# Kernel optimization log

Hardware: AMD Instinct MI355X
Metric: run time of the kernel (lower is better)

Reference implementation:

```python
import jax, jax.numpy as jnp
import numpy as np

DIM = 768
HEADS = 12
HEAD_DIM = DIM // HEADS
SCALE = HEAD_DIM ** -0.5


def setup_inputs() -> dict:
    key = jax.random.key(0)
    k1, k2, k3, k4 = jax.random.split(key, 4)
    x = jax.random.normal(k1, (8, 1025, DIM), dtype=jnp.float32)
    # torch nn.Linear weight layout: (out_features, in_features)
    w_qkv = jax.random.normal(k2, (3 * DIM, DIM), dtype=jnp.float32) * (DIM ** -0.5)
    w_proj = jax.random.normal(k3, (DIM, DIM), dtype=jnp.float32) * (DIM ** -0.5)
    b_proj = jax.random.normal(k4, (DIM,), dtype=jnp.float32) * 0.01
    return {"x": x, "w_qkv": w_qkv, "w_proj": w_proj, "b_proj": b_proj}


def reference(x, w_qkv, w_proj, b_proj):
    B, N, C = x.shape
    H, D = HEADS, HEAD_DIM
    # qkv: (B, N, 3C) -> (3, B, H, N, D)
    qkv = jnp.einsum('bnc,oc->bno', x, w_qkv)
    qkv = qkv.reshape(B, N, 3, H, D).transpose(2, 0, 3, 1, 4)
    q, k, v = qkv[0], qkv[1], qkv[2]
    attn = jnp.einsum('bhnd,bhmd->bhnm', q, k) * SCALE
    attn = jax.nn.softmax(attn, axis=-1)
    out = jnp.einsum('bhnm,bhmd->bhnd', attn, v)
    out = out.transpose(0, 2, 1, 3).reshape(B, N, C)
    out = jnp.einsum('bnc,oc->bno', out, w_proj) + b_proj
    return out
```

## Files before the change

kernel.cpp:

```cpp
#include <hip/hip_runtime.h>
#include <stdint.h>

#define DIMC 768
#define NSEQ 1025
#define BATCH 8
#define HEADS 12
#define HDIM 64
#define OC3 2304
#define MROWS (BATCH * NSEQ)
#define NBH (BATCH * HEADS)
#define KVB 64
#define NT 17
#define QTILE 128
#define NQT 9
#define HTILES 9
#define VSTRIDE (NT * KVB)
#define C2 0.1803368801111244f
#define OFFB (-11.541560327111707f)

typedef short bf16x8 __attribute__((ext_vector_type(8)));
typedef float f32x4 __attribute__((ext_vector_type(4)));
typedef float f32x16 __attribute__((ext_vector_type(16)));
typedef uint32_t u32x4 __attribute__((ext_vector_type(4)));

__device__ __forceinline__ uint32_t f2bf(float x) {
    uint32_t u = __builtin_bit_cast(uint32_t, x);
    return (u + 0x7fffu + ((u >> 16) & 1u)) >> 16;
}
__device__ __forceinline__ float bf2f(uint32_t b) {
    return __builtin_bit_cast(float, b << 16);
}
__device__ __forceinline__ float4 ld4(const float* p) {
    return *reinterpret_cast<const float4*>(p);
}
__device__ __forceinline__ uint32_t cvtpk(float lo, float hi) {
    uint32_t r;
    asm("v_cvt_pk_bf16_f32 %0, %1, %2" : "=v"(r) : "v"(lo), "v"(hi));
    return r;
}
__device__ __forceinline__ void plswap(uint32_t& x, uint32_t& y) {
    asm volatile("v_permlane32_swap_b32 %0, %1" : "+v"(x), "+v"(y));
}
__device__ __forceinline__ void async_cp16(void* lds, const void* g) {
    __builtin_amdgcn_global_load_lds(
        (const __attribute__((address_space(1))) uint32_t*)g,
        (__attribute__((address_space(3))) uint32_t*)lds, 16, 0, 0);
}

__global__ __launch_bounds__(256) void cvt_all(const float* __restrict__ x,
                                               const float* __restrict__ wq,
                                               const float* __restrict__ wp,
                                               uint16_t* __restrict__ xb,
                                               uint16_t* __restrict__ wqb,
                                               uint16_t* __restrict__ wpb) {
    const int NX = MROWS * DIMC / 8, NQ = OC3 * DIMC / 8, NP = DIMC * DIMC / 8;
    const int i = blockIdx.x * 256 + threadIdx.x;
    const float* src;
    uint16_t* dst;
    int off;
    if (i < NX)                { src = x;  dst = xb;  off = i; }
    else if (i < NX + NQ)      { src = wq; dst = wqb; off = i - NX; }
    else if (i < NX + NQ + NP) { src = wp; dst = wpb; off = i - NX - NQ; }
    else return;
    const float4 a = ld4(src + off * 8), b = ld4(src + off * 8 + 4);
    uint4 o;
    o.x = f2bf(a.x) | (f2bf(a.y) << 16);
    o.y = f2bf(a.z) | (f2bf(a.w) << 16);
    o.z = f2bf(b.x) | (f2bf(b.y) << 16);
    o.w = f2bf(b.z) | (f2bf(b.w) << 16);
    *reinterpret_cast<uint4*>(dst + off * 8) = o;
}

template <bool OUTBF, bool BIAS>
__global__ __launch_bounds__(256) void gemm_bf16_nt(const uint16_t* __restrict__ A,
                                                    const uint16_t* __restrict__ W,
                                                    const float* __restrict__ bias,
                                                    void* __restrict__ Out,
                                                    int M, int N, int K) {
    __shared__ __align__(16) char smem[32768];
    char* const As = smem;
    char* const Ws = smem + 16384;

    const int tid = threadIdx.x;
    const int wave = tid >> 6, lane = tid & 63;
    const int l15 = lane & 15, l4 = lane >> 4;
    const int wr = wave >> 1, wc = wave & 1;
    const int m0 = blockIdx.y * 128, n0 = blockIdx.x * 128;

    f32x4 acc[4][4] = {};

    int srow[4], scol[4];
#pragma unroll
    for (int i = 0; i < 4; ++i) {
        const int X = i * 4096 + wave * 1024 + lane * 16;
        const int row = X >> 7;
        const int slot = (X & 127) >> 4;
        srow[i] = row;
        scol[i] = (slot ^ (row & 7)) << 3;
    }

    for (int kt = 0; kt < K; kt += 64) {
        __syncthreads();
#pragma unroll
        for (int i = 0; i < 4; ++i) {
            int am = m0 + srow[i];
            if (am >= M) am = M - 1;
            async_cp16(As + i * 4096 + wave * 1024,
                       A + (size_t)am * K + kt + scol[i]);
            const int wn = n0 + srow[i];
            async_cp16(Ws + i * 4096 + wave * 1024,
                       W + (size_t)wn * K + kt + scol[i]);
        }
        __syncthreads();

#pragma unroll
        for (int ch = 0; ch < 2; ++ch) {
            const int kb = (ch << 6) + (l4 << 4);
            bf16x8 af[4], bw[4];
#pragma unroll
            for (int mi = 0; mi < 4; ++mi) {
                const int row = wr * 64 + mi * 16 + l15;
                af[mi] = *(const bf16x8*)(As + (row << 7) + (kb ^ ((row & 7) << 4)));
            }
#pragma unroll
            for (int nj = 0; nj < 4; ++nj) {
                const int row = wc * 64 + nj * 16 + l15;
                bw[nj] = *(const bf16x8*)(Ws + (row << 7) + (kb ^ ((row & 7) << 4)));
            }
#pragma unroll
            for (int mi = 0; mi < 4; ++mi)
#pragma unroll
                for (int nj = 0; nj < 4; ++nj)
                    acc[mi][nj] = __builtin_amdgcn_mfma_f32_16x16x32_bf16(
                        af[mi], bw[nj], acc[mi][nj], 0, 0, 0);
        }
    }

#pragma unroll
    for (int mi = 0; mi < 4; ++mi) {
#pragma unroll
        for (int r = 0; r < 4; ++r) {
            const int m = m0 + wr * 64 + mi * 16 + l4 * 4 + r;
            if (m < M) {
#pragma unroll
                for (int nj = 0; nj < 4; ++nj) {
                    const int n = n0 + wc * 64 + nj * 16 + l15;
                    float v = acc[mi][nj][r];
                    if (BIAS) v += bias[n];
                    if (OUTBF)
                        ((uint16_t*)Out)[(size_t)m * N + n] = (uint16_t)f2bf(v);
                    else
                        ((float*)Out)[(size_t)m * N + n] = v;
                }
            }
        }
    }
}

__global__ __launch_bounds__(256) void vtrans(const uint16_t* __restrict__ qkv,
                                              uint16_t* __restrict__ vt) {
    const int kt = blockIdx.x, bh = blockIdx.y;
    const int h = bh % HEADS, b = bh / HEADS;
    __shared__ __align__(16) char lds[8192];
    const int tid = threadIdx.x;
    const uint16_t* src = qkv + (size_t)b * NSEQ * OC3 + 2 * DIMC + h * HDIM;
    uint16_t* dst = vt + (size_t)bh * HDIM * VSTRIDE + kt * KVB;

#pragma unroll
    for (int i = 0; i < 2; ++i) {
        const int s = i * 256 + tid;
        const int kv = s >> 3, c = s & 7;
        int kvg = kt * KVB + kv;
        if (kvg > NSEQ - 1) kvg = NSEQ - 1;
        const uint4 d4 = *(const uint4*)(src + (size_t)kvg * OC3 + c * 8);
        *(uint4*)(lds + (kv << 7) + ((c ^ (kv & 7)) << 4)) = d4;
    }
    __syncthreads();

#pragma unroll
    for (int i = 0; i < 2; ++i) {
        const int s = i * 256 + tid;
        const int d = s >> 3, c = s & 7;
        uint32_t w[4];
#pragma unroll
        for (int p = 0; p < 4; ++p) {
            const int k0 = c * 8 + p * 2, k1 = k0 + 1;
            const uint32_t lo = *(const uint16_t*)(lds + (k0 << 7) +
                ((((d >> 3) ^ (k0 & 7)) << 4) + ((d & 7) << 1)));
            const uint32_t hi = *(const uint16_t*)(lds + (k1 << 7) +
                ((((d >> 3) ^ (k1 & 7)) << 4) + ((d & 7) << 1)));
            w[p] = lo | (hi << 16);
        }
        uint4 o4;
        o4.x = w[0]; o4.y = w[1]; o4.z = w[2]; o4.w = w[3];
        *(uint4*)(dst + (size_t)d * VSTRIDE + c * 8) = o4;
    }
}

__global__ __launch_bounds__(256) void flash_attn2(const uint16_t* __restrict__ qkv,
                                                   const uint16_t* __restrict__ vt,
                                                   uint16_t* __restrict__ opart,
                                                   float* __restrict__ lpart) {
    const int wg = blockIdx.x;
    const int lg = (wg & 7) * 216 + (wg >> 3);
    const int qt = lg % NQT;
    const int g = lg / NQT;
    const int bh = g >> 1;
    const int half = g & 1;
    const int h = bh % HEADS, b = bh / HEADS;

    const int tid = threadIdx.x;
    const int wave = tid >> 6, lane = tid & 63;
    const int l31 = lane & 31, lh = lane >> 5;

    __shared__ __align__(16) char smem[32768];

    const uint16_t* Kg = qkv + (size_t)b * NSEQ * OC3 + DIMC + h * HDIM;
    const uint16_t* Vt = vt + (size_t)bh * HDIM * VSTRIDE;

    bf16x8 qf[4];
    {
        int qrow = qt * QTILE + wave * 32 + l31;
        if (qrow > NSEQ - 1) qrow = NSEQ - 1;
        const uint16_t* Qg = qkv + (size_t)(b * NSEQ + qrow) * OC3 + h * HDIM;
#pragma unroll
        for (int ds = 0; ds < 4; ++ds)
            qf[ds] = *(const bf16x8*)(Qg + ds * 16 + lh * 8);
    }

    bf16x8 ones;
#pragma unroll
    for (int i = 0; i < 8; ++i) ones[i] = (short)0x3F80;

    auto stageK = [&](int kv0, char* Kb) {
#pragma unroll
        for (int i = 0; i < 2; ++i) {
            const int X = i * 4096 + wave * 1024 + lane * 16;
            const int row = X >> 7;
            const int slot = (X & 127) >> 4;
            int kvg = kv0 + row;
            if (kvg > NSEQ - 1) kvg = NSEQ - 1;
            async_cp16(Kb + i * 4096 + wave * 1024,
                       Kg + (size_t)kvg * OC3 + ((slot ^ (row & 7)) << 3));
        }
    };
    auto stageV = [&](int kv0, char* Vb) {
#pragma unroll
        for (int i = 0; i < 2; ++i) {
            const int X = i * 4096 + wave * 1024 + lane * 16;
            const int d = X >> 7;
            const int slot = (X & 127) >> 4;
            async_cp16(Vb + i * 4096 + wave * 1024,
                       Vt + (size_t)d * VSTRIDE + kv0 + ((slot ^ (d & 7)) << 3));
        }
    };

    const int tstart = half * HTILES;
    const int tend = half ? NT : HTILES;

    stageK(tstart * KVB, smem);
    stageV(tstart * KVB, smem + 16384);
    __syncthreads();

    f32x16 o[2] = {};
    f32x16 osum = {};

    for (int t = tstart; t < tend; ++t) {
        const int cur = (t - tstart) & 1;
        const int kv0 = t * KVB;
        char* const Kc = smem + cur * 8192;
        char* const Vc = smem + 16384 + cur * 8192;

        if (t < tend - 1) {
            stageK(kv0 + KVB, smem + (cur ^ 1) * 8192);
            stageV(kv0 + KVB, smem + 16384 + (cur ^ 1) * 8192);
        }

        f32x16 s[2] = {};
        __builtin_amdgcn_s_setprio(1);
#pragma unroll
        for (int kvb = 0; kvb < 2; ++kvb) {
            const int krow = kvb * 32 + l31;
            const int kbase = (krow << 7);
            const int sw = (l31 & 7) << 4;
#pragma unroll
            for (int ds = 0; ds < 4; ++ds) {
                bf16x8 kf = *(const bf16x8*)(Kc + kbase + ((ds * 32 + lh * 16) ^ sw));
                s[kvb] = __builtin_amdgcn_mfma_f32_32x32x16_bf16(kf, qf[ds], s[kvb], 0, 0, 0);
            }
        }
        __builtin_amdgcn_s_setprio(0);

        if (t == NT - 1) {
#pragma unroll
            for (int kvb = 0; kvb < 2; ++kvb)
#pragma unroll
                for (int r = 0; r < 16; ++r) {
                    const int kvg = kv0 + kvb * 32 + (r & 3) + 8 * (r >> 2) + 4 * lh;
                    if (kvg >= NSEQ) s[kvb][r] = -INFINITY;
                }
        }

#pragma unroll
        for (int kvb = 0; kvb < 2; ++kvb)
#pragma unroll
            for (int r = 0; r < 16; ++r)
                s[kvb][r] = __builtin_amdgcn_exp2f(fmaf(s[kvb][r], C2, OFFB));

        bf16x8 pa[4];
#pragma unroll
        for (int kb = 0; kb < 4; ++kb) {
            const f32x16 S = s[kb >> 1];
            const int c = (kb & 1) * 8;
            uint32_t w0 = cvtpk(S[c + 0], S[c + 1]);
            uint32_t w2 = cvtpk(S[c + 4], S[c + 5]);
            plswap(w0, w2);
            uint32_t w1 = cvtpk(S[c + 2], S[c + 3]);
            uint32_t w3 = cvtpk(S[c + 6], S[c + 7]);
            plswap(w1, w3);
            u32x4 w;
            w[0] = w0; w[1] = w1; w[2] = w2; w[3] = w3;
            pa[kb] = __builtin_bit_cast(bf16x8, w);
        }

        __builtin_amdgcn_s_setprio(1);
#pragma unroll
        for (int kb = 0; kb < 4; ++kb)
            osum = __builtin_amdgcn_mfma_f32_32x32x16_bf16(ones, pa[kb], osum, 0, 0, 0);
#pragma unroll
        for (int db = 0; db < 2; ++db) {
            const int d = db * 32 + l31;
            const int dbase = (d << 7);
            const int sw = (l31 & 7) << 4;
#pragma unroll
            for (int kb = 0; kb < 4; ++kb) {
                bf16x8 vf = *(const bf16x8*)(Vc + dbase + ((kb * 32 + lh * 16) ^ sw));
                o[db] = __builtin_amdgcn_mfma_f32_32x32x16_bf16(vf, pa[kb], o[db], 0, 0, 0);
            }
        }
        __builtin_amdgcn_s_setprio(0);

        if (t < tend - 1) __syncthreads();
    }

    {
        const int qrow = qt * QTILE + wave * 32 + l31;
        if (qrow < NSEQ) {
            const size_t row = ((size_t)half * NBH + bh) * NSEQ + qrow;
            uint16_t* orow = opart + row * HDIM;
#pragma unroll
            for (int db = 0; db < 2; ++db)
#pragma unroll
                for (int g4 = 0; g4 < 4; ++g4) {
                    const int d = db * 32 + g4 * 8 + lh * 4;
                    uint2 ww;
                    ww.x = cvtpk(o[db][g4 * 4 + 0], o[db][g4 * 4 + 1]);
                    ww.y = cvtpk(o[db][g4 * 4 + 2], o[db][g4 * 4 + 3]);
                    *(uint2*)(orow + d) = ww;
                }
            if (lh == 0) lpart[row] = osum[0];
        }
    }
}

__global__ __launch_bounds__(256) void combine(const uint16_t* __restrict__ opart,
                                               const float* __restrict__ lpart,
                                               uint16_t* __restrict__ attb) {
    const int gid = blockIdx.x * 256 + threadIdx.x;
    if (gid >= NBH * NSEQ * 8) return;
    const int oct = gid & 7;
    const int t = gid >> 3;
    const int bh = t / NSEQ;
    const int q = t - bh * NSEQ;
    const int h = bh % HEADS, b = bh / HEADS;
    const size_t HALF = (size_t)NBH * NSEQ;

    const uint4 o1 = *(const uint4*)(opart + (size_t)t * HDIM + oct * 8);
    const uint4 o2 = *(const uint4*)(opart + (HALF + t) * HDIM + oct * 8);
    const float inv = 1.0f / (lpart[t] + lpart[HALF + t]);

    const uint32_t a[4] = {o1.x, o1.y, o1.z, o1.w};
    const uint32_t c[4] = {o2.x, o2.y, o2.z, o2.w};
    uint2 w0, w1;
    float v[8];
#pragma unroll
    for (int p = 0; p < 4; ++p) {
        v[p * 2 + 0] = (bf2f(a[p] & 0xffffu) + bf2f(c[p] & 0xffffu)) * inv;
        v[p * 2 + 1] = (bf2f(a[p] >> 16) + bf2f(c[p] >> 16)) * inv;
    }
    w0.x = cvtpk(v[0], v[1]); w0.y = cvtpk(v[2], v[3]);
    w1.x = cvtpk(v[4], v[5]); w1.y = cvtpk(v[6], v[7]);

    uint16_t* dst = attb + ((size_t)b * NSEQ + q) * DIMC + h * HDIM + oct * 8;
    *(uint2*)dst = w0;
    *(uint2*)(dst + 4) = w1;
}

extern "C" void kernel_launch(void* const* d_in, const int* in_sizes, int n_in,
                              void* d_out, int out_size, void* d_ws, size_t ws_size,
                              hipStream_t stream) {
    const float* x      = (const float*)d_in[0];
    const float* w_qkv  = (const float*)d_in[1];
    const float* w_proj = (const float*)d_in[2];
    const float* b_proj = (const float*)d_in[3];
    float* out = (float*)d_out;

    const size_t NVT = (size_t)NBH * HDIM * VSTRIDE;
    const size_t NOP = (size_t)2 * NBH * NSEQ * HDIM;
    uint16_t* xb    = (uint16_t*)d_ws;
    uint16_t* wqb   = xb  + (size_t)MROWS * DIMC;
    uint16_t* wpb   = wqb + (size_t)OC3 * DIMC;
    uint16_t* qkv   = wpb + (size_t)DIMC * DIMC;
    uint16_t* vt    = qkv + (size_t)MROWS * OC3;
    uint16_t* opart = vt + NVT;
    float*    lpart = (float*)(opart + NOP);
    uint16_t* attb  = (uint16_t*)(lpart + (size_t)2 * NBH * NSEQ);

    const dim3 blk(256);
    const int ncvt = (MROWS * DIMC + OC3 * DIMC + DIMC * DIMC) / 8;
    cvt_all<<<dim3((ncvt + 255) / 256), blk, 0, stream>>>(x, w_qkv, w_proj, xb, wqb, wpb);

    gemm_bf16_nt<true, false><<<dim3(OC3 / 128, (MROWS + 127) / 128), blk, 0, stream>>>(
        xb, wqb, nullptr, qkv, MROWS, OC3, DIMC);

    vtrans<<<dim3(NT, NBH), blk, 0, stream>>>(qkv, vt);

    flash_attn2<<<dim3(NQT * NBH * 2), blk, 0, stream>>>(qkv, vt, opart, lpart);

    combine<<<dim3((NBH * NSEQ * 8 + 255) / 256), blk, 0, stream>>>(opart, lpart, attb);

    gemm_bf16_nt<false, true><<<dim3(DIMC / 128, (MROWS + 127) / 128), blk, 0, stream>>>(
        attb, wpb, b_proj, out, MROWS, DIMC, DIMC);
}
```

Baseline: 136.1 us.

## Process two 32-row query groups per wave with 128-thread attention blocks

The flash attention kernel now runs 2 waves per block instead of 4, and each wave handles 64 query rows as two 32-row groups. Each K and V fragment read from LDS therefore feeds two MFMAs, halving LDS reads per unit of compute. Staging loops are widened so the two waves still fill the same 128-row tile. The cost is roughly double the accumulator registers per wave and fewer waves per block, which may lower occupancy and reduce latency hiding.

```diff
diff --git a/kernel.cpp b/kernel.cpp
--- a/kernel.cpp
+++ b/kernel.cpp
@@ -197,7 +197,7 @@
     }
 }
 
-__global__ __launch_bounds__(256) void flash_attn2(const uint16_t* __restrict__ qkv,
+__global__ __launch_bounds__(128) void flash_attn2(const uint16_t* __restrict__ qkv,
                                                    const uint16_t* __restrict__ vt,
                                                    uint16_t* __restrict__ opart,
                                                    float* __restrict__ lpart) {
@@ -218,14 +218,15 @@
     const uint16_t* Kg = qkv + (size_t)b * NSEQ * OC3 + DIMC + h * HDIM;
     const uint16_t* Vt = vt + (size_t)bh * HDIM * VSTRIDE;
 
-    bf16x8 qf[4];
-    {
-        int qrow = qt * QTILE + wave * 32 + l31;
+    bf16x8 qf[2][4];
+#pragma unroll
+    for (int G = 0; G < 2; ++G) {
+        int qrow = qt * QTILE + wave * 64 + G * 32 + l31;
         if (qrow > NSEQ - 1) qrow = NSEQ - 1;
         const uint16_t* Qg = qkv + (size_t)(b * NSEQ + qrow) * OC3 + h * HDIM;
 #pragma unroll
         for (int ds = 0; ds < 4; ++ds)
-            qf[ds] = *(const bf16x8*)(Qg + ds * 16 + lh * 8);
+            qf[G][ds] = *(const bf16x8*)(Qg + ds * 16 + lh * 8);
     }
 
     bf16x8 ones;
@@ -234,23 +235,23 @@
 
     auto stageK = [&](int kv0, char* Kb) {
 #pragma unroll
-        for (int i = 0; i < 2; ++i) {
-            const int X = i * 4096 + wave * 1024 + lane * 16;
+        for (int i = 0; i < 4; ++i) {
+            const int X = i * 2048 + wave * 1024 + lane * 16;
             const int row = X >> 7;
             const int slot = (X & 127) >> 4;
             int kvg = kv0 + row;
             if (kvg > NSEQ - 1) kvg = NSEQ - 1;
-            async_cp16(Kb + i * 4096 + wave * 1024,
+            async_cp16(Kb + i * 2048 + wave * 1024,
                        Kg + (size_t)kvg * OC3 + ((slot ^ (row & 7)) << 3));
         }
     };
     auto stageV = [&](int kv0, char* Vb) {
 #pragma unroll
-        for (int i = 0; i < 2; ++i) {
-            const int X = i * 4096 + wave * 1024 + lane * 16;
+        for (int i = 0; i < 4; ++i) {
+            const int X = i * 2048 + wave * 1024 + lane * 16;
             const int d = X >> 7;
             const int slot = (X & 127) >> 4;
-            async_cp16(Vb + i * 4096 + wave * 1024,
+            async_cp16(Vb + i * 2048 + wave * 1024,
                        Vt + (size_t)d * VSTRIDE + kv0 + ((slot ^ (d & 7)) << 3));
         }
     };
@@ -262,8 +263,8 @@
     stageV(tstart * KVB, smem + 16384);
     __syncthreads();
 
-    f32x16 o[2] = {};
-    f32x16 osum = {};
+    f32x16 o[2][2] = {};
+    f32x16 osum[2] = {};
 
     for (int t = tstart; t < tend; ++t) {
         const int cur = (t - tstart) & 1;
@@ -276,7 +277,7 @@
             stageV(kv0 + KVB, smem + 16384 + (cur ^ 1) * 8192);
         }
 
-        f32x16 s[2] = {};
+        f32x16 s[2][2] = {};
         __builtin_amdgcn_s_setprio(1);
 #pragma unroll
         for (int kvb = 0; kvb < 2; ++kvb) {
@@ -286,47 +287,56 @@
 #pragma unroll
             for (int ds = 0; ds < 4; ++ds) {
                 bf16x8 kf = *(const bf16x8*)(Kc + kbase + ((ds * 32 + lh * 16) ^ sw));
-                s[kvb] = __builtin_amdgcn_mfma_f32_32x32x16_bf16(kf, qf[ds], s[kvb], 0, 0, 0);
+                s[0][kvb] = __builtin_amdgcn_mfma_f32_32x32x16_bf16(kf, qf[0][ds], s[0][kvb], 0, 0, 0);
+                s[1][kvb] = __builtin_amdgcn_mfma_f32_32x32x16_bf16(kf, qf[1][ds], s[1][kvb], 0, 0, 0);
             }
         }
         __builtin_amdgcn_s_setprio(0);
 
         if (t == NT - 1) {
 #pragma unroll
+            for (int G = 0; G < 2; ++G)
+#pragma unroll
+                for (int kvb = 0; kvb < 2; ++kvb)
+#pragma unroll
+                    for (int r = 0; r < 16; ++r) {
+                        const int kvg = kv0 + kvb * 32 + (r & 3) + 8 * (r >> 2) + 4 * lh;
+                        if (kvg >= NSEQ) s[G][kvb][r] = -INFINITY;
+                    }
+        }
+
+#pragma unroll
+        for (int G = 0; G < 2; ++G)
+#pragma unroll
             for (int kvb = 0; kvb < 2; ++kvb)
 #pragma unroll
-                for (int r = 0; r < 16; ++r) {
-                    const int kvg = kv0 + kvb * 32 + (r & 3) + 8 * (r >> 2) + 4 * lh;
-                    if (kvg >= NSEQ) s[kvb][r] = -INFINITY;
-                }
-        }
-
-#pragma unroll
-        for (int kvb = 0; kvb < 2; ++kvb)
-#pragma unroll
-            for (int r = 0; r < 16; ++r)
-                s[kvb][r] = __builtin_amdgcn_exp2f(fmaf(s[kvb][r], C2, OFFB));
-
-        bf16x8 pa[4];
+                for (int r = 0; r < 16; ++r)
+                    s[G][kvb][r] = __builtin_amdgcn_exp2f(fmaf(s[G][kvb][r], C2, OFFB));
+
+        bf16x8 pa[2][4];
+#pragma unroll
+        for (int G = 0; G < 2; ++G)
+#pragma unroll
+            for (int kb = 0; kb < 4; ++kb) {
+                const f32x16 S = s[G][kb >> 1];
+                const int c = (kb & 1) * 8;
+                uint32_t w0 = cvtpk(S[c + 0], S[c + 1]);
+                uint32_t w2 = cvtpk(S[c + 4], S[c + 5]);
+                plswap(w0, w2);
+                uint32_t w1 = cvtpk(S[c + 2], S[c + 3]);
+                uint32_t w3 = cvtpk(S[c + 6], S[c + 7]);
+                plswap(w1, w3);
+                u32x4 w;
+                w[0] = w0; w[1] = w1; w[2] = w2; w[3] = w3;
+                pa[G][kb] = __builtin_bit_cast(bf16x8, w);
+            }
+
+        __builtin_amdgcn_s_setprio(1);
 #pragma unroll
         for (int kb = 0; kb < 4; ++kb) {
-            const f32x16 S = s[kb >> 1];
-            const int c = (kb & 1) * 8;
-            uint32_t w0 = cvtpk(S[c + 0], S[c + 1]);
-            uint32_t w2 = cvtpk(S[c + 4], S[c + 5]);
-            plswap(w0, w2);
-            uint32_t w1 = cvtpk(S[c + 2], S[c + 3]);
-            uint32_t w3 = cvtpk(S[c + 6], S[c + 7]);
-            plswap(w1, w3);
-            u32x4 w;
-            w[0] = w0; w[1] = w1; w[2] = w2; w[3] = w3;
-            pa[kb] = __builtin_bit_cast(bf16x8, w);
-        }
-
-        __builtin_amdgcn_s_setprio(1);
-#pragma unroll
-        for (int kb = 0; kb < 4; ++kb)
-            osum = __builtin_amdgcn_mfma_f32_32x32x16_bf16(ones, pa[kb], osum, 0, 0, 0);
+            osum[0] = __builtin_amdgcn_mfma_f32_32x32x16_bf16(ones, pa[0][kb], osum[0], 0, 0, 0);
+            osum[1] = __builtin_amdgcn_mfma_f32_32x32x16_bf16(ones, pa[1][kb], osum[1], 0, 0, 0);
+        }
 #pragma unroll
         for (int db = 0; db < 2; ++db) {
             const int d = db * 32 + l31;
@@ -335,7 +345,8 @@
 #pragma unroll
             for (int kb = 0; kb < 4; ++kb) {
                 bf16x8 vf = *(const bf16x8*)(Vc + dbase + ((kb * 32 + lh * 16) ^ sw));
-                o[db] = __builtin_amdgcn_mfma_f32_32x32x16_bf16(vf, pa[kb], o[db], 0, 0, 0);
+                o[0][db] = __builtin_amdgcn_mfma_f32_32x32x16_bf16(vf, pa[0][kb], o[0][db], 0, 0, 0);
+                o[1][db] = __builtin_amdgcn_mfma_f32_32x32x16_bf16(vf, pa[1][kb], o[1][db], 0, 0, 0);
             }
         }
         __builtin_amdgcn_s_setprio(0);
@@ -343,8 +354,9 @@
         if (t < tend - 1) __syncthreads();
     }
 
-    {
-        const int qrow = qt * QTILE + wave * 32 + l31;
+#pragma unroll
+    for (int G = 0; G < 2; ++G) {
+        const int qrow = qt * QTILE + wave * 64 + G * 32 + l31;
         if (qrow < NSEQ) {
             const size_t row = ((size_t)half * NBH + bh) * NSEQ + qrow;
             uint16_t* orow = opart + row * HDIM;
@@ -354,11 +366,11 @@
                 for (int g4 = 0; g4 < 4; ++g4) {
                     const int d = db * 32 + g4 * 8 + lh * 4;
                     uint2 ww;
-                    ww.x = cvtpk(o[db][g4 * 4 + 0], o[db][g4 * 4 + 1]);
-                    ww.y = cvtpk(o[db][g4 * 4 + 2], o[db][g4 * 4 + 3]);
+                    ww.x = cvtpk(o[G][db][g4 * 4 + 0], o[G][db][g4 * 4 + 1]);
+                    ww.y = cvtpk(o[G][db][g4 * 4 + 2], o[G][db][g4 * 4 + 3]);
                     *(uint2*)(orow + d) = ww;
                 }
-            if (lh == 0) lpart[row] = osum[0];
+            if (lh == 0) lpart[row] = osum[G][0];
         }
     }
 }
@@ -425,7 +437,7 @@
 
     vtrans<<<dim3(NT, NBH), blk, 0, stream>>>(qkv, vt);
 
-    flash_attn2<<<dim3(NQT * NBH * 2), blk, 0, stream>>>(qkv, vt, opart, lpart);
+    flash_attn2<<<dim3(NQT * NBH * 2), dim3(128), 0, stream>>>(qkv, vt, opart, lpart);
 
     combine<<<dim3((NBH * NSEQ * 8 + 255) / 256), blk, 0, stream>>>(opart, lpart, attb);
 
```

New measurement: 158.3 us. +16.3%, slower.
